# Optimization experiments

Measured on AMD Instinct MI355X. Metric: run time of the kernel, lower is better.

## Reference

```python
import jax, jax.numpy as jnp
import numpy as np
import math

B, S, H, D = 8, 2048, 1024, 64  # batch, seq_len, hidden_dim, head_size

def setup_inputs() -> dict:
    key = jax.random.key(0)
    ks = jax.random.split(key, 7)
    lim = 1.0 / math.sqrt(H)  # torch Linear default init bound
    return {
        "x":  jax.random.normal(ks[0], (B, S, H), dtype=jnp.float32),
        "Wq": jax.random.uniform(ks[1], (H, D), jnp.float32, -lim, lim),
        "bq": jax.random.uniform(ks[2], (D,),   jnp.float32, -lim, lim),
        "Wk": jax.random.uniform(ks[3], (H, D), jnp.float32, -lim, lim),
        "bk": jax.random.uniform(ks[4], (D,),   jnp.float32, -lim, lim),
        "Wv": jax.random.uniform(ks[5], (H, D), jnp.float32, -lim, lim),
        "bv": jax.random.uniform(ks[6], (D,),   jnp.float32, -lim, lim),
    }

def reference(x, Wq, bq, Wk, bk, Wv, bv):
    # x: [B, S, H]
    q = x @ Wq + bq          # [B, S, D]
    k = x @ Wk + bk          # [B, S, D]
    v = x @ Wv + bv          # [B, S, D]
    scores = jnp.einsum("bsd,btd->bst", q, k)       # [B, S, S]
    causal = jnp.tril(jnp.ones((S, S), dtype=bool))
    scores = jnp.where(causal, scores, -jnp.inf)
    # NOTE: original module (faithfully) applies softmax FIRST, then divides
    # by sqrt(hidden_dim) -- it does NOT scale logits before softmax.
    weight = jax.nn.softmax(scores, axis=-1) / jnp.sqrt(jnp.float32(x.shape[-1]))
    # dropout p=0.0 -> identity
    return jnp.einsum("bst,btd->bsd", weight, v)     # [B, S, D]
```

## Files before the change

kernel.cpp:

```cpp
#include <hip/hip_runtime.h>


typedef float     f32x4 __attribute__((ext_vector_type(4)));
typedef _Float16  f16x8 __attribute__((ext_vector_type(8)));
typedef _Float16  f16x4 __attribute__((ext_vector_type(4)));

__device__ __forceinline__ float wave_max16(float v) {
  #pragma unroll
  for (int off = 1; off < 16; off <<= 1) v = fmaxf(v, __shfl_xor(v, off, 64));
  return v;
}
__device__ __forceinline__ float wave_sum16(float v) {
  #pragma unroll
  for (int off = 1; off < 16; off <<= 1) v += __shfl_xor(v, off, 64);
  return v;
}

__global__ __launch_bounds__(256) void wt_prep(const float* __restrict__ Wq,
                                               const float* __restrict__ Wk,
                                               const float* __restrict__ Wv,
                                               _Float16* __restrict__ WtF) {
  const int w  = blockIdx.x >> 4;
  const int kt = blockIdx.x & 15;
  const float* src = (w == 0) ? Wq : (w == 1 ? Wk : Wv);
  __shared__ _Float16 ls[64][72];
  const int t = threadIdx.x;
  {
    int rr = t >> 4;
    int c4 = (t & 15) * 4;
    #pragma unroll
    for (int ri = 0; ri < 4; ++ri) {
      int k = rr + ri * 16;
      f32x4 f = *(const f32x4*)&src[(size_t)(kt * 64 + k) * 64 + c4];
      #pragma unroll
      for (int j = 0; j < 4; ++j) ls[k][c4 + j] = (_Float16)f[j];
    }
  }
  __syncthreads();
  const int lane = t & 63, l16 = lane & 15, quad = lane >> 4;
  #pragma unroll
  for (int h = 0; h < 2; ++h) {
    int fid     = h * 4 + (t >> 6);
    int kstep_l = fid >> 2;
    int ntl     = fid & 3;
    int nt      = w * 4 + ntl;
    int kstep   = kt * 2 + kstep_l;
    f16x8 o;
    #pragma unroll
    for (int j = 0; j < 8; ++j) o[j] = ls[kstep_l * 32 + quad * 8 + j][ntl * 16 + l16];
    *(f16x8*)&WtF[((size_t)(kstep * 12 + nt) * 64 + lane) * 8] = o;
  }
}

__global__ __launch_bounds__(512, 4) void qkv_gemm(const float* __restrict__ x,
                                                   const _Float16* __restrict__ WtF,
                                                   const float* __restrict__ bq,
                                                   const float* __restrict__ bk,
                                                   const float* __restrict__ bv,
                                                   _Float16* __restrict__ qo,
                                                   _Float16* __restrict__ ko,
                                                   _Float16* __restrict__ vt) {
  __shared__ _Float16 xs[32 * 1024];
  const int tid  = threadIdx.x;
  const int wave = tid >> 6, lane = tid & 63;
  const int l16  = lane & 15, quad = lane >> 4;
  const int mhalf = wave >> 2;
  const int ngrp  = wave & 3;
  const int m0    = blockIdx.x * 32;

  {
    int row   = tid >> 4;
    int cbase = (tid & 15) * 4;
    const float* xrow = x + (size_t)(m0 + row) * 1024;
    int key = row & 7;
    #pragma unroll
    for (int j = 0; j < 16; ++j) {
      int col = cbase + j * 64;
      f32x4 f = *(const f32x4*)&xrow[col];
      f16x4 hh;
      #pragma unroll
      for (int e = 0; e < 4; ++e) hh[e] = (_Float16)f[e];
      int g   = col >> 3;
      int sub = col & 7;
      *(f16x4*)&xs[(size_t)row * 1024 + (size_t)((g ^ key) << 3) + sub] = hh;
    }
  }
  __syncthreads();

  f32x4 acc0 = (f32x4){0.f,0.f,0.f,0.f};
  f32x4 acc1 = (f32x4){0.f,0.f,0.f,0.f};
  f32x4 acc2 = (f32x4){0.f,0.f,0.f,0.f};

  const int arow = mhalf * 16 + l16;
  const _Float16* abase = xs + (size_t)arow * 1024;
  const int akey = arow & 7;
  const _Float16* wbase = WtF + ((size_t)(ngrp * 3) * 64 + lane) * 8;

  #pragma unroll 4
  for (int kstep = 0; kstep < 32; ++kstep) {
    f16x8 a = *(const f16x8*)(abase + (((kstep * 4 + quad) ^ akey) << 3));
    const _Float16* wk = wbase + (size_t)kstep * (12 * 64 * 8);
    f16x8 b0 = *(const f16x8*)(wk);
    f16x8 b1 = *(const f16x8*)(wk + 512);
    f16x8 b2 = *(const f16x8*)(wk + 1024);
    acc0 = __builtin_amdgcn_mfma_f32_16x16x32_f16(a, b0, acc0, 0, 0, 0);
    acc1 = __builtin_amdgcn_mfma_f32_16x16x32_f16(a, b1, acc1, 0, 0, 0);
    acc2 = __builtin_amdgcn_mfma_f32_16x16x32_f16(a, b2, acc2, 0, 0, 0);
  }

  f32x4 accs[3] = {acc0, acc1, acc2};
  #pragma unroll
  for (int i = 0; i < 3; ++i) {
    int nt  = ngrp * 3 + i;
    int col = nt * 16 + l16;
    float bias = (nt < 4) ? bq[col] : (nt < 8) ? bk[col - 64] : bv[col - 128];
    #pragma unroll
    for (int r = 0; r < 4; ++r) {
      int m = m0 + mhalf * 16 + quad * 4 + r;
      _Float16 hv = (_Float16)(accs[i][r] + bias);
      if (nt < 4)      qo[(size_t)m * 64 + col] = hv;
      else if (nt < 8) ko[(size_t)m * 64 + (col - 64)] = hv;
      else {
        int b = m >> 11, s = m & 2047;
        vt[((size_t)b * 64 + (col - 128)) * 2048 + s] = hv;
      }
    }
  }
}

__global__ __launch_bounds__(256) void attn(const _Float16* __restrict__ q,
                                            const _Float16* __restrict__ k,
                                            const _Float16* __restrict__ vt,
                                            float* __restrict__ out) {
  const int blk  = blockIdx.x;
  const int qt   = 127 - (blk >> 3);
  const int b    = blk & 7;
  const int tid  = threadIdx.x;
  const int wave = tid >> 6, lane = tid & 63;
  const int l16  = lane & 15, quad = lane >> 4;
  const int q0   = qt * 16;

  __shared__ _Float16 P[4][16][72];
  __shared__ float    ob[4][16][66];
  __shared__ float    mlb[4][2][16];

  const _Float16* qb = q  + (size_t)b * 2048 * 64;
  const _Float16* kb = k  + (size_t)b * 2048 * 64;
  const _Float16* vb = vt + (size_t)b * 64 * 2048;

  f16x8 qf0 = *(const f16x8*)&qb[(q0 + l16) * 64 + quad * 8];
  f16x8 qf1 = *(const f16x8*)&qb[(q0 + l16) * 64 + 32 + quad * 8];

  f32x4 o[4];
  #pragma unroll
  for (int i = 0; i < 4; ++i) o[i] = (f32x4){0.f, 0.f, 0.f, 0.f};
  float mrow[4] = {-1e30f, -1e30f, -1e30f, -1e30f};
  float lrow[4] = {0.f, 0.f, 0.f, 0.f};
  const float L2E = 1.44269504088896340736f;

  const int kvend = q0 + 16;
  for (int kv0 = wave * 64; kv0 < kvend; kv0 += 256) {
    f32x4 sc[4];
    #pragma unroll
    for (int t = 0; t < 4; ++t) {
      int kvc = kv0 + t * 16;
      f32x4 c = (f32x4){0.f, 0.f, 0.f, 0.f};
      if (kvc < kvend) {
        f16x8 kf0 = *(const f16x8*)&kb[(kvc + l16) * 64 + quad * 8];
        f16x8 kf1 = *(const f16x8*)&kb[(kvc + l16) * 64 + 32 + quad * 8];
        c = __builtin_amdgcn_mfma_f32_16x16x32_f16(qf0, kf0, c, 0, 0, 0);
        c = __builtin_amdgcn_mfma_f32_16x16x32_f16(qf1, kf1, c, 0, 0, 0);
      }
      sc[t] = c;
    }
    if (kv0 + 63 > q0) {
      #pragma unroll
      for (int t = 0; t < 4; ++t) {
        int skv = kv0 + t * 16 + l16;
        #pragma unroll
        for (int r = 0; r < 4; ++r) {
          int sq = q0 + quad * 4 + r;
          if (skv > sq) sc[t][r] = -1e30f;
        }
      }
    }
    float alpha[4];
    #pragma unroll
    for (int r = 0; r < 4; ++r) {
      float mx = fmaxf(fmaxf(sc[0][r], sc[1][r]), fmaxf(sc[2][r], sc[3][r]));
      mx = wave_max16(mx);
      float mnew = fmaxf(mrow[r], mx);
      alpha[r] = exp2f((mrow[r] - mnew) * L2E);
      mrow[r] = mnew;
    }
    #pragma unroll
    for (int t = 0; t < 4; ++t)
      #pragma unroll
      for (int r = 0; r < 4; ++r)
        sc[t][r] = exp2f((sc[t][r] - mrow[r]) * L2E);
    #pragma unroll
    for (int r = 0; r < 4; ++r) {
      float s = sc[0][r] + sc[1][r] + sc[2][r] + sc[3][r];
      s = wave_sum16(s);
      lrow[r] = lrow[r] * alpha[r] + s;
      #pragma unroll
      for (int dt = 0; dt < 4; ++dt) o[dt][r] *= alpha[r];
    }
    #pragma unroll
    for (int t = 0; t < 4; ++t)
      #pragma unroll
      for (int r = 0; r < 4; ++r)
        P[wave][quad * 4 + r][t * 16 + l16] = (_Float16)sc[t][r];
    asm volatile("s_waitcnt lgkmcnt(0)" ::: "memory");
    f16x8 p0 = *(const f16x8*)&P[wave][l16][quad * 8];
    f16x8 p1 = *(const f16x8*)&P[wave][l16][32 + quad * 8];
    #pragma unroll
    for (int dt = 0; dt < 4; ++dt) {
      f16x8 v0 = *(const f16x8*)&vb[(size_t)(dt * 16 + l16) * 2048 + kv0 + quad * 8];
      f16x8 v1 = *(const f16x8*)&vb[(size_t)(dt * 16 + l16) * 2048 + kv0 + 32 + quad * 8];
      o[dt] = __builtin_amdgcn_mfma_f32_16x16x32_f16(p0, v0, o[dt], 0, 0, 0);
      o[dt] = __builtin_amdgcn_mfma_f32_16x16x32_f16(p1, v1, o[dt], 0, 0, 0);
    }
  }

  #pragma unroll
  for (int dt = 0; dt < 4; ++dt)
    #pragma unroll
    for (int r = 0; r < 4; ++r)
      ob[wave][quad * 4 + r][dt * 16 + l16] = o[dt][r];
  if (l16 == 0) {
    #pragma unroll
    for (int r = 0; r < 4; ++r) {
      mlb[wave][0][quad * 4 + r] = mrow[r];
      mlb[wave][1][quad * 4 + r] = lrow[r];
    }
  }
  __syncthreads();

  {
    int row = tid >> 4;
    int c0  = (tid & 15) * 4;
    float m0 = mlb[0][0][row], m1 = mlb[1][0][row];
    float m2 = mlb[2][0][row], m3 = mlb[3][0][row];
    float M  = fmaxf(fmaxf(m0, m1), fmaxf(m2, m3));
    float w0 = exp2f((m0 - M) * L2E), w1 = exp2f((m1 - M) * L2E);
    float w2 = exp2f((m2 - M) * L2E), w3 = exp2f((m3 - M) * L2E);
    float L  = w0 * mlb[0][1][row] + w1 * mlb[1][1][row]
             + w2 * mlb[2][1][row] + w3 * mlb[3][1][row];
    float inv = 1.0f / (L * 32.0f);
    f32x4 res;
    #pragma unroll
    for (int j = 0; j < 4; ++j)
      res[j] = (w0 * ob[0][row][c0 + j] + w1 * ob[1][row][c0 + j]
              + w2 * ob[2][row][c0 + j] + w3 * ob[3][row][c0 + j]) * inv;
    *(f32x4*)&out[((size_t)b * 2048 + q0 + row) * 64 + c0] = res;
  }
}

extern "C" void kernel_launch(void* const* d_in, const int* in_sizes, int n_in,
                              void* d_out, int out_size, void* d_ws, size_t ws_size,
                              hipStream_t stream) {
  const float* x  = (const float*)d_in[0];
  const float* Wq = (const float*)d_in[1];
  const float* bq = (const float*)d_in[2];
  const float* Wk = (const float*)d_in[3];
  const float* bk = (const float*)d_in[4];
  const float* Wv = (const float*)d_in[5];
  const float* bv = (const float*)d_in[6];
  float* out = (float*)d_out;

  _Float16* WtF = (_Float16*)d_ws;
  _Float16* qo  = WtF + 192 * 1024;
  _Float16* ko  = qo + 16384 * 64;
  _Float16* vt  = ko + 16384 * 64;

  hipLaunchKernelGGL(wt_prep,  dim3(48),   dim3(256), 0, stream, Wq, Wk, Wv, WtF);
  hipLaunchKernelGGL(qkv_gemm, dim3(512),  dim3(512), 0, stream, x, WtF, bq, bk, bv, qo, ko, vt);
  hipLaunchKernelGGL(attn,     dim3(1024), dim3(256), 0, stream, qo, ko, vt, out);
}
```

Baseline: 156.2 us.

## Split attention over KV chunks with separate merge kernel; widen QKV GEMM blocks

The attention kernel becomes split-KV. Each block handles one 16-row query tile and one 256-key chunk, mapped through a triangular index so no block is idle. It writes fp16 partial outputs plus per-row max and sum to workspace, and a new merge kernel combines them. The QK and PV MMAs are transposed so each lane owns one query row, which replaces the 16-lane shuffle reductions with two cross-quad shuffles. The QKV GEMM moves to 768 threads with two N-tiles per wave instead of three. The aim is to fix load imbalance and the long serial KV loop in the causal attention, at the cost of an extra launch, partial-result traffic, and fp16 rounding of the partials.

```diff
diff --git a/kernel.cpp b/kernel.cpp
--- a/kernel.cpp
+++ b/kernel.cpp
@@ -5,16 +5,7 @@
 typedef _Float16  f16x8 __attribute__((ext_vector_type(8)));
 typedef _Float16  f16x4 __attribute__((ext_vector_type(4)));
 
-__device__ __forceinline__ float wave_max16(float v) {
-  #pragma unroll
-  for (int off = 1; off < 16; off <<= 1) v = fmaxf(v, __shfl_xor(v, off, 64));
-  return v;
-}
-__device__ __forceinline__ float wave_sum16(float v) {
-  #pragma unroll
-  for (int off = 1; off < 16; off <<= 1) v += __shfl_xor(v, off, 64);
-  return v;
-}
+#define L2E 1.44269504088896340736f
 
 __global__ __launch_bounds__(256) void wt_prep(const float* __restrict__ Wq,
                                                const float* __restrict__ Wk,
@@ -52,23 +43,23 @@
   }
 }
 
-__global__ __launch_bounds__(512, 4) void qkv_gemm(const float* __restrict__ x,
-                                                   const _Float16* __restrict__ WtF,
-                                                   const float* __restrict__ bq,
-                                                   const float* __restrict__ bk,
-                                                   const float* __restrict__ bv,
-                                                   _Float16* __restrict__ qo,
-                                                   _Float16* __restrict__ ko,
-                                                   _Float16* __restrict__ vt) {
+__global__ __launch_bounds__(768) void qkv_gemm(const float* __restrict__ x,
+                                                const _Float16* __restrict__ WtF,
+                                                const float* __restrict__ bq,
+                                                const float* __restrict__ bk,
+                                                const float* __restrict__ bv,
+                                                _Float16* __restrict__ qo,
+                                                _Float16* __restrict__ ko,
+                                                _Float16* __restrict__ vt) {
   __shared__ _Float16 xs[32 * 1024];
   const int tid  = threadIdx.x;
   const int wave = tid >> 6, lane = tid & 63;
   const int l16  = lane & 15, quad = lane >> 4;
-  const int mhalf = wave >> 2;
-  const int ngrp  = wave & 3;
+  const int mhalf = wave / 6;
+  const int ngrp  = wave - mhalf * 6;
   const int m0    = blockIdx.x * 32;
 
-  {
+  if (tid < 512) {
     int row   = tid >> 4;
     int cbase = (tid & 15) * 4;
     const float* xrow = x + (size_t)(m0 + row) * 1024;
@@ -89,12 +80,10 @@
 
   f32x4 acc0 = (f32x4){0.f,0.f,0.f,0.f};
   f32x4 acc1 = (f32x4){0.f,0.f,0.f,0.f};
-  f32x4 acc2 = (f32x4){0.f,0.f,0.f,0.f};
-
   const int arow = mhalf * 16 + l16;
   const _Float16* abase = xs + (size_t)arow * 1024;
   const int akey = arow & 7;
-  const _Float16* wbase = WtF + ((size_t)(ngrp * 3) * 64 + lane) * 8;
+  const _Float16* wbase = WtF + ((size_t)(ngrp * 2) * 64 + lane) * 8;
 
   #pragma unroll 4
   for (int kstep = 0; kstep < 32; ++kstep) {
@@ -102,16 +91,14 @@
     const _Float16* wk = wbase + (size_t)kstep * (12 * 64 * 8);
     f16x8 b0 = *(const f16x8*)(wk);
     f16x8 b1 = *(const f16x8*)(wk + 512);
-    f16x8 b2 = *(const f16x8*)(wk + 1024);
     acc0 = __builtin_amdgcn_mfma_f32_16x16x32_f16(a, b0, acc0, 0, 0, 0);
     acc1 = __builtin_amdgcn_mfma_f32_16x16x32_f16(a, b1, acc1, 0, 0, 0);
-    acc2 = __builtin_amdgcn_mfma_f32_16x16x32_f16(a, b2, acc2, 0, 0, 0);
-  }
-
-  f32x4 accs[3] = {acc0, acc1, acc2};
-  #pragma unroll
-  for (int i = 0; i < 3; ++i) {
-    int nt  = ngrp * 3 + i;
+  }
+
+  f32x4 accs[2] = {acc0, acc1};
+  #pragma unroll
+  for (int i = 0; i < 2; ++i) {
+    int nt  = ngrp * 2 + i;
     int col = nt * 16 + l16;
     float bias = (nt < 4) ? bq[col] : (nt < 8) ? bk[col - 64] : bv[col - 128];
     #pragma unroll
@@ -131,130 +118,151 @@
 __global__ __launch_bounds__(256) void attn(const _Float16* __restrict__ q,
                                             const _Float16* __restrict__ k,
                                             const _Float16* __restrict__ vt,
-                                            float* __restrict__ out) {
-  const int blk  = blockIdx.x;
-  const int qt   = 127 - (blk >> 3);
-  const int b    = blk & 7;
+                                            _Float16* __restrict__ po,
+                                            float* __restrict__ pm,
+                                            float* __restrict__ pl) {
+  const int bid = 575 - blockIdx.x;
+  const int b   = blockIdx.y;
+  int g = 0;
+  #pragma unroll
+  for (int gg = 0; gg < 7; ++gg) if (bid >= 8 * (gg + 1) * (gg + 2)) g = gg + 1;
+  const int r   = bid - 8 * g * (g + 1);
+  const int qi  = r / (g + 1);
+  const int qt  = 16 * g + qi;
+  const int s   = r - qi * (g + 1);
+  const int q0  = qt * 16, kvend = q0 + 16;
+
   const int tid  = threadIdx.x;
   const int wave = tid >> 6, lane = tid & 63;
   const int l16  = lane & 15, quad = lane >> 4;
-  const int q0   = qt * 16;
-
-  __shared__ _Float16 P[4][16][72];
-  __shared__ float    ob[4][16][66];
-  __shared__ float    mlb[4][2][16];
-
-  const _Float16* qb = q  + (size_t)b * 2048 * 64;
-  const _Float16* kb = k  + (size_t)b * 2048 * 64;
-  const _Float16* vb = vt + (size_t)b * 64 * 2048;
-
-  f16x8 qf0 = *(const f16x8*)&qb[(q0 + l16) * 64 + quad * 8];
-  f16x8 qf1 = *(const f16x8*)&qb[(q0 + l16) * 64 + 32 + quad * 8];
-
+  const int kv0  = s * 256 + wave * 64;
+
+  __shared__ float ow[4][64][17];
+  __shared__ float mw[4][16], lw[4][16];
+  _Float16* Plw = (_Float16*)&ow[wave][0][0];
+
+  float m = -1e30f, l = 0.f;
   f32x4 o[4];
   #pragma unroll
   for (int i = 0; i < 4; ++i) o[i] = (f32x4){0.f, 0.f, 0.f, 0.f};
-  float mrow[4] = {-1e30f, -1e30f, -1e30f, -1e30f};
-  float lrow[4] = {0.f, 0.f, 0.f, 0.f};
-  const float L2E = 1.44269504088896340736f;
-
-  const int kvend = q0 + 16;
-  for (int kv0 = wave * 64; kv0 < kvend; kv0 += 256) {
+
+  if (kv0 < kvend) {
+    const _Float16* qb = q  + (size_t)b * 2048 * 64;
+    const _Float16* kb = k  + (size_t)b * 2048 * 64;
+    const _Float16* vb = vt + (size_t)b * 64 * 2048;
+    f16x8 qf0 = *(const f16x8*)&qb[(q0 + l16) * 64 + quad * 8];
+    f16x8 qf1 = *(const f16x8*)&qb[(q0 + l16) * 64 + 32 + quad * 8];
+
     f32x4 sc[4];
     #pragma unroll
     for (int t = 0; t < 4; ++t) {
       int kvc = kv0 + t * 16;
-      f32x4 c = (f32x4){0.f, 0.f, 0.f, 0.f};
       if (kvc < kvend) {
         f16x8 kf0 = *(const f16x8*)&kb[(kvc + l16) * 64 + quad * 8];
         f16x8 kf1 = *(const f16x8*)&kb[(kvc + l16) * 64 + 32 + quad * 8];
-        c = __builtin_amdgcn_mfma_f32_16x16x32_f16(qf0, kf0, c, 0, 0, 0);
-        c = __builtin_amdgcn_mfma_f32_16x16x32_f16(qf1, kf1, c, 0, 0, 0);
-      }
-      sc[t] = c;
+        f32x4 c = (f32x4){0.f, 0.f, 0.f, 0.f};
+        c = __builtin_amdgcn_mfma_f32_16x16x32_f16(kf0, qf0, c, 0, 0, 0);
+        c = __builtin_amdgcn_mfma_f32_16x16x32_f16(kf1, qf1, c, 0, 0, 0);
+        sc[t] = c;
+      } else sc[t] = (f32x4){-1e30f, -1e30f, -1e30f, -1e30f};
     }
     if (kv0 + 63 > q0) {
       #pragma unroll
       for (int t = 0; t < 4; ++t) {
-        int skv = kv0 + t * 16 + l16;
         #pragma unroll
-        for (int r = 0; r < 4; ++r) {
-          int sq = q0 + quad * 4 + r;
-          if (skv > sq) sc[t][r] = -1e30f;
+        for (int rr = 0; rr < 4; ++rr) {
+          int skv = kv0 + t * 16 + quad * 4 + rr;
+          if (skv > q0 + l16) sc[t][rr] = -1e30f;
         }
       }
     }
-    float alpha[4];
-    #pragma unroll
-    for (int r = 0; r < 4; ++r) {
-      float mx = fmaxf(fmaxf(sc[0][r], sc[1][r]), fmaxf(sc[2][r], sc[3][r]));
-      mx = wave_max16(mx);
-      float mnew = fmaxf(mrow[r], mx);
-      alpha[r] = exp2f((mrow[r] - mnew) * L2E);
-      mrow[r] = mnew;
-    }
+    float mx = sc[0][0];
     #pragma unroll
     for (int t = 0; t < 4; ++t)
       #pragma unroll
-      for (int r = 0; r < 4; ++r)
-        sc[t][r] = exp2f((sc[t][r] - mrow[r]) * L2E);
-    #pragma unroll
-    for (int r = 0; r < 4; ++r) {
-      float s = sc[0][r] + sc[1][r] + sc[2][r] + sc[3][r];
-      s = wave_sum16(s);
-      lrow[r] = lrow[r] * alpha[r] + s;
-      #pragma unroll
-      for (int dt = 0; dt < 4; ++dt) o[dt][r] *= alpha[r];
-    }
+      for (int rr = 0; rr < 4; ++rr) mx = fmaxf(mx, sc[t][rr]);
+    mx = fmaxf(mx, __shfl_xor(mx, 16, 64));
+    mx = fmaxf(mx, __shfl_xor(mx, 32, 64));
+    m = mx;
+    float sum = 0.f;
     #pragma unroll
     for (int t = 0; t < 4; ++t)
       #pragma unroll
-      for (int r = 0; r < 4; ++r)
-        P[wave][quad * 4 + r][t * 16 + l16] = (_Float16)sc[t][r];
+      for (int rr = 0; rr < 4; ++rr) {
+        float e = exp2f((sc[t][rr] - m) * L2E);
+        sc[t][rr] = e;
+        sum += e;
+      }
+    sum += __shfl_xor(sum, 16, 64);
+    sum += __shfl_xor(sum, 32, 64);
+    l = sum;
+    #pragma unroll
+    for (int t = 0; t < 4; ++t)
+      #pragma unroll
+      for (int rr = 0; rr < 4; ++rr)
+        Plw[l16 * 72 + t * 16 + quad * 4 + rr] = (_Float16)sc[t][rr];
     asm volatile("s_waitcnt lgkmcnt(0)" ::: "memory");
-    f16x8 p0 = *(const f16x8*)&P[wave][l16][quad * 8];
-    f16x8 p1 = *(const f16x8*)&P[wave][l16][32 + quad * 8];
+    f16x8 p0 = *(const f16x8*)&Plw[l16 * 72 + quad * 8];
+    f16x8 p1 = *(const f16x8*)&Plw[l16 * 72 + 32 + quad * 8];
     #pragma unroll
     for (int dt = 0; dt < 4; ++dt) {
       f16x8 v0 = *(const f16x8*)&vb[(size_t)(dt * 16 + l16) * 2048 + kv0 + quad * 8];
       f16x8 v1 = *(const f16x8*)&vb[(size_t)(dt * 16 + l16) * 2048 + kv0 + 32 + quad * 8];
-      o[dt] = __builtin_amdgcn_mfma_f32_16x16x32_f16(p0, v0, o[dt], 0, 0, 0);
-      o[dt] = __builtin_amdgcn_mfma_f32_16x16x32_f16(p1, v1, o[dt], 0, 0, 0);
-    }
-  }
-
+      o[dt] = __builtin_amdgcn_mfma_f32_16x16x32_f16(v0, p0, o[dt], 0, 0, 0);
+      o[dt] = __builtin_amdgcn_mfma_f32_16x16x32_f16(v1, p1, o[dt], 0, 0, 0);
+    }
+  }
+
+  __syncthreads();
   #pragma unroll
   for (int dt = 0; dt < 4; ++dt)
     #pragma unroll
-    for (int r = 0; r < 4; ++r)
-      ob[wave][quad * 4 + r][dt * 16 + l16] = o[dt][r];
-  if (l16 == 0) {
-    #pragma unroll
-    for (int r = 0; r < 4; ++r) {
-      mlb[wave][0][quad * 4 + r] = mrow[r];
-      mlb[wave][1][quad * 4 + r] = lrow[r];
-    }
-  }
+    for (int rr = 0; rr < 4; ++rr)
+      ow[wave][dt * 16 + quad * 4 + rr][l16] = o[dt][rr];
+  if (quad == 0) { mw[wave][l16] = m; lw[wave][l16] = l; }
   __syncthreads();
 
   {
-    int row = tid >> 4;
-    int c0  = (tid & 15) * 4;
-    float m0 = mlb[0][0][row], m1 = mlb[1][0][row];
-    float m2 = mlb[2][0][row], m3 = mlb[3][0][row];
-    float M  = fmaxf(fmaxf(m0, m1), fmaxf(m2, m3));
-    float w0 = exp2f((m0 - M) * L2E), w1 = exp2f((m1 - M) * L2E);
-    float w2 = exp2f((m2 - M) * L2E), w3 = exp2f((m3 - M) * L2E);
-    float L  = w0 * mlb[0][1][row] + w1 * mlb[1][1][row]
-             + w2 * mlb[2][1][row] + w3 * mlb[3][1][row];
-    float inv = 1.0f / (L * 32.0f);
-    f32x4 res;
+    int qrow = tid >> 4, d4 = (tid & 15) * 4;
+    float m0v = mw[0][qrow], m1v = mw[1][qrow], m2v = mw[2][qrow], m3v = mw[3][qrow];
+    float M = fmaxf(fmaxf(m0v, m1v), fmaxf(m2v, m3v));
+    float w0 = exp2f((m0v - M) * L2E), w1 = exp2f((m1v - M) * L2E);
+    float w2 = exp2f((m2v - M) * L2E), w3 = exp2f((m3v - M) * L2E);
+    float L = w0 * lw[0][qrow] + w1 * lw[1][qrow] + w2 * lw[2][qrow] + w3 * lw[3][qrow];
+    size_t pid = (size_t)b * 576 + bid;
+    f16x4 oh;
     #pragma unroll
     for (int j = 0; j < 4; ++j)
-      res[j] = (w0 * ob[0][row][c0 + j] + w1 * ob[1][row][c0 + j]
-              + w2 * ob[2][row][c0 + j] + w3 * ob[3][row][c0 + j]) * inv;
-    *(f32x4*)&out[((size_t)b * 2048 + q0 + row) * 64 + c0] = res;
-  }
+      oh[j] = (_Float16)(w0 * ow[0][d4 + j][qrow] + w1 * ow[1][d4 + j][qrow]
+                       + w2 * ow[2][d4 + j][qrow] + w3 * ow[3][d4 + j][qrow]);
+    *(f16x4*)&po[pid * 1024 + (size_t)qrow * 64 + d4] = oh;
+    if ((tid & 15) == 0) { pm[pid * 16 + qrow] = M; pl[pid * 16 + qrow] = L; }
+  }
+}
+
+__global__ __launch_bounds__(256) void attn_merge(const _Float16* __restrict__ po,
+                                                  const float* __restrict__ pm,
+                                                  const float* __restrict__ pl,
+                                                  float* __restrict__ out) {
+  const int qt = blockIdx.x, b = blockIdx.y;
+  const int g = qt >> 4, S = g + 1;
+  const size_t base = (size_t)b * 576 + (size_t)(g + 1) * (8 * g + (qt & 15));
+  const int t = threadIdx.x, qrow = t >> 4, d4 = (t & 15) * 4;
+
+  float M = -1e30f;
+  for (int s = 0; s < S; ++s) M = fmaxf(M, pm[(base + s) * 16 + qrow]);
+  float L = 0.f;
+  float O0 = 0.f, O1 = 0.f, O2 = 0.f, O3 = 0.f;
+  for (int s = 0; s < S; ++s) {
+    float w = exp2f((pm[(base + s) * 16 + qrow] - M) * L2E);
+    L += w * pl[(base + s) * 16 + qrow];
+    f16x4 ov = *(const f16x4*)&po[(base + s) * 1024 + (size_t)qrow * 64 + d4];
+    O0 += w * (float)ov[0]; O1 += w * (float)ov[1];
+    O2 += w * (float)ov[2]; O3 += w * (float)ov[3];
+  }
+  float inv = 1.0f / (L * 32.0f);
+  f32x4 res = (f32x4){O0 * inv, O1 * inv, O2 * inv, O3 * inv};
+  *(f32x4*)&out[((size_t)b * 2048 + qt * 16 + qrow) * 64 + d4] = res;
 }
 
 extern "C" void kernel_launch(void* const* d_in, const int* in_sizes, int n_in,
@@ -273,8 +281,12 @@
   _Float16* qo  = WtF + 192 * 1024;
   _Float16* ko  = qo + 16384 * 64;
   _Float16* vt  = ko + 16384 * 64;
-
-  hipLaunchKernelGGL(wt_prep,  dim3(48),   dim3(256), 0, stream, Wq, Wk, Wv, WtF);
-  hipLaunchKernelGGL(qkv_gemm, dim3(512),  dim3(512), 0, stream, x, WtF, bq, bk, bv, qo, ko, vt);
-  hipLaunchKernelGGL(attn,     dim3(1024), dim3(256), 0, stream, qo, ko, vt, out);
-}
+  _Float16* po  = vt + 8 * 64 * 2048;
+  float*    pm  = (float*)(po + (size_t)4608 * 1024);
+  float*    pl  = pm + 4608 * 16;
+
+  hipLaunchKernelGGL(wt_prep,    dim3(48),       dim3(256), 0, stream, Wq, Wk, Wv, WtF);
+  hipLaunchKernelGGL(qkv_gemm,   dim3(512),      dim3(768), 0, stream, x, WtF, bq, bk, bv, qo, ko, vt);
+  hipLaunchKernelGGL(attn,       dim3(576, 8),   dim3(256), 0, stream, qo, ko, vt, po, pm, pl);
+  hipLaunchKernelGGL(attn_merge, dim3(128, 8),   dim3(256), 0, stream, po, pm, pl, out);
+}
```

Measured after the change: 162.9 us. 1.04x slower.
